# Performance work log

Hardware: AMD Instinct MI355X
Metric: run time of the kernel (lower is better)

## Reference

```python
import jax, jax.numpy as jnp
import numpy as np

NB = 31      # num_bands
PD = 64      # processing_dim


def _conv(x, w, b, groups, pad):
    # x: NCHW, w: OIHW (I = in_channels/groups)
    y = jax.lax.conv_general_dilated(
        x, w, window_strides=(1, 1), padding=pad,
        feature_group_count=groups,
        dimension_numbers=('NCHW', 'OIHW', 'NCHW'))
    return y + b[None, :, None, None]


def _gelu(z):
    # torch.nn.GELU() default is exact (erf-based)
    return jax.nn.gelu(z, approximate=False)


def setup_inputs() -> dict:
    key = jax.random.key(0)
    ks = jax.random.split(key, 11)
    s = 0.05
    inp = {
        'x':   jax.random.normal(ks[0], (2, NB, 192, 192), dtype=jnp.float32),
        # 31 independent band processors, stacked as grouped-conv weights (groups=31)
        'W1':  jax.random.normal(ks[1], (NB * PD, 1, 3, 3), dtype=jnp.float32) * s,
        'b1':  jax.random.normal(ks[2], (NB * PD,), dtype=jnp.float32) * s,
        'W2':  jax.random.normal(ks[3], (NB * PD, PD, 3, 3), dtype=jnp.float32) * s,
        'b2':  jax.random.normal(ks[4], (NB * PD,), dtype=jnp.float32) * s,
        'W3':  jax.random.normal(ks[5], (NB, PD, 1, 1), dtype=jnp.float32) * s,
        'b3':  jax.random.normal(ks[6], (NB,), dtype=jnp.float32) * s,
        # cross-band fusion 1x1 convs
        'Wf1': jax.random.normal(ks[7], (NB * 2, NB, 1, 1), dtype=jnp.float32) * s,
        'bf1': jax.random.normal(ks[8], (NB * 2,), dtype=jnp.float32) * s,
        'Wf2': jax.random.normal(ks[9], (NB, NB * 2, 1, 1), dtype=jnp.float32) * s,
        'bf2': jax.random.normal(ks[10], (NB,), dtype=jnp.float32) * s,
    }
    return inp


def reference(x, W1, b1, W2, b2, W3, b3, Wf1, bf1, Wf2, bf2):
    P3 = [(1, 1), (1, 1)]
    P1 = [(0, 0), (0, 0)]
    # per-band 3-layer stacks expressed as grouped convs (groups = num_bands)
    h = _gelu(_conv(x, W1, b1, NB, P3))           # [B, 31*64, H, W]
    h = _gelu(_conv(h, W2, b2, NB, P3))           # [B, 31*64, H, W]
    processed = _conv(h, W3, b3, NB, P1)          # [B, 31, H, W]
    # cross-band fusion
    f = _gelu(_conv(processed, Wf1, bf1, 1, P1))  # [B, 62, H, W]
    fused = _conv(f, Wf2, bf2, 1, P1)             # [B, 31, H, W]
    return x + fused
```

## Files before the change

kernel.cpp:

```cpp
#include <hip/hip_runtime.h>
#include <hip/hip_bf16.h>

#define NB 31
#define PD 64

typedef __attribute__((ext_vector_type(8))) short short8;
typedef __attribute__((ext_vector_type(16))) float f32x16;
typedef __attribute__((ext_vector_type(8))) int int8v;

__device__ __forceinline__ float gelu_f(float x) {
    float y = x * x;
    float p = __builtin_fmaf(y, __builtin_fmaf(y, 0.0042294f, -0.056913f), 0.395442f);
    float phi;
    asm("v_fma_f32 %0, %1, %2, 0.5 clamp" : "=v"(phi) : "v"(x), "v"(p));
    return x * phi;
}

__device__ __forceinline__ unsigned int cvt_pk_bf16(float lo, float hi) {
    unsigned int r;
    asm("v_cvt_pk_bf16_f32 %0, %1, %2" : "=v"(r) : "v"(lo), "v"(hi));
    return r;
}

__device__ __forceinline__ unsigned int pk_fp8(float a, float b) {
    return (unsigned int)__builtin_amdgcn_cvt_pk_fp8_f32(a, b, 0, false);
}

__device__ __forceinline__ int8v mk8(uint4 a, uint4 b) {
    int8v r;
    r[0] = a.x; r[1] = a.y; r[2] = a.z; r[3] = a.w;
    r[4] = b.x; r[5] = b.y; r[6] = b.z; r[7] = b.w;
    return r;
}

__global__ void prep_w2(const float* __restrict__ W2, unsigned char* __restrict__ W2s) {
    int e = blockIdx.x * 256 + threadIdx.x;
    const int TOT = NB * 2 * 9 * 64;
    if (e >= TOT) return;
    int lane = e & 63;
    int tap  = (e >> 6) % 9;
    int gh   = e / (9 * 64);
    int g = gh >> 1, oh = gh & 1;
    int col = lane & 31, hi = lane >> 5;
    const float* wp = W2 + ((size_t)(g * 64 + oh * 32 + col) * 64 + hi * 32) * 9 + tap;
    unsigned int d[8];
#pragma unroll
    for (int i = 0; i < 8; ++i) {
        float f0 = wp[(4 * i + 0) * 9];
        float f1 = wp[(4 * i + 1) * 9];
        float f2 = wp[(4 * i + 2) * 9];
        float f3 = wp[(4 * i + 3) * 9];
        d[i] = pk_fp8(f0, f1) | (pk_fp8(f2, f3) << 16);
    }
    uint4 q0, q1;
    q0.x = d[0]; q0.y = d[2]; q0.z = d[1]; q0.w = d[3];
    q1.x = d[4]; q1.y = d[6]; q1.z = d[5]; q1.w = d[7];
    uint4* op = (uint4*)W2s + (size_t)e * 2;
    op[0] = q0; op[1] = q1;
}

__global__ __launch_bounds__(512, 5) void band_kernel(
    const float* __restrict__ x, const float* __restrict__ W1, const float* __restrict__ b1,
    const float* __restrict__ b2, const float* __restrict__ W3, const float* __restrict__ b3,
    const unsigned char* __restrict__ W2s, float* __restrict__ out)
{
    __shared__ float xs[20 * 20];
    __shared__ uint4 h1s[352 * 5];
    __shared__ float outs[2 * 256];

    const int tid = threadIdx.x;
    const int tx = blockIdx.x % 12, ty = blockIdx.x / 12;
    const int g = blockIdx.y, n = blockIdx.z;
    const int x0 = tx * 16, y0 = ty * 16;

    const int lane = tid & 63;
    const int wid  = tid >> 6;
    const int w4   = wid & 3;
    const int oh   = wid >> 2;
    const int hi   = lane >> 5;
    const int col  = lane & 31;

    const float* xg = x + (size_t)(n * NB + g) * 192 * 192;
    if (tid < 400) {
        int r = tid / 20, c = tid - r * 20;
        int gy = y0 + r - 2, gx = x0 + c - 2;
        float v = 0.f;
        if (gy >= 0 && gy < 192 && gx >= 0 && gx < 192) v = xg[gy * 192 + gx];
        xs[tid] = v;
    }

    short8 a1;
    {
        const float* wp = W1 + (size_t)(g * 64 + oh * 32 + col) * 9;
        uint4 bw = {0u, 0u, 0u, 0u};
        if (hi == 0) {
            bw.x = cvt_pk_bf16(wp[0], wp[1]);
            bw.y = cvt_pk_bf16(wp[2], wp[3]);
            bw.z = cvt_pk_bf16(wp[4], wp[5]);
            bw.w = cvt_pk_bf16(wp[6], wp[7]);
        } else {
            bw.x = cvt_pk_bf16(wp[8], b1[g * 64 + oh * 32 + col]);
        }
        a1 = __builtin_bit_cast(short8, bw);
    }
    __syncthreads();

    char* h1c = (char*)h1s;
#pragma unroll
    for (int it = 0; it < 3; ++it) {
        const int t = w4 + 4 * it;
        if (t < 11) {
            const int posr = t * 32 + col;
            const int pos  = posr < 324 ? posr : 323;
            int py = pos / 18, px = pos - py * 18;
            int gy = y0 + py - 1, gx = x0 + px - 1;
            unsigned int msk = (gy >= 0 && gy < 192 && gx >= 0 && gx < 192) ? 0xFFFFFFFFu : 0u;

            uint4 bw = {0u, 0u, 0u, 0u};
            if (hi == 0) {
                float xv[8];
#pragma unroll
                for (int j2 = 0; j2 < 8; ++j2)
                    xv[j2] = xs[(py + j2 / 3) * 20 + px + (j2 % 3)];
                bw.x = cvt_pk_bf16(xv[0], xv[1]);
                bw.y = cvt_pk_bf16(xv[2], xv[3]);
                bw.z = cvt_pk_bf16(xv[4], xv[5]);
                bw.w = cvt_pk_bf16(xv[6], xv[7]);
            } else {
                bw.x = cvt_pk_bf16(xs[(py + 2) * 20 + px + 2], 1.0f);
            }
            short8 bfrag = __builtin_bit_cast(short8, bw);

            f32x16 z = {};
            f32x16 c0 = __builtin_amdgcn_mfma_f32_32x32x16_bf16(a1, bfrag, z, 0, 0, 0);

            const int rowb = posr * 80;
#pragma unroll
            for (int p2 = 0; p2 < 2; ++p2) {
                const int s0 = 2 * p2, s1 = 2 * p2 + 1;
                float u0 = gelu_f(c0[4 * s0 + 0]);
                float u1 = gelu_f(c0[4 * s0 + 1]);
                float u2 = gelu_f(c0[4 * s0 + 2]);
                float u3 = gelu_f(c0[4 * s0 + 3]);
                float v0 = gelu_f(c0[4 * s1 + 0]);
                float v1 = gelu_f(c0[4 * s1 + 1]);
                float v2 = gelu_f(c0[4 * s1 + 2]);
                float v3 = gelu_f(c0[4 * s1 + 3]);
                uint2 st;
                st.x = (pk_fp8(u0, u1) | (pk_fp8(u2, u3) << 16)) & msk;
                st.y = (pk_fp8(v0, v1) | (pk_fp8(v2, v3) << 16)) & msk;
                *(uint2*)(h1c + rowb + ((2 * oh + p2) << 4) + (hi << 3)) = st;
            }
        }
    }
    __syncthreads();

    const int lhalf = (lane >> 4) & 1;
    const int pxl   = lane & 15;
    const int base0 = (4 * w4 + lhalf) * 18 + pxl;

    const int gh = g * 2 + oh;
    const uint4* ap = (const uint4*)W2s + (size_t)gh * 9 * 128 + lane * 2;

    f32x16 acc0, acc1;
    {
        const float* bp = b2 + g * 64 + oh * 32 + 4 * hi;
#pragma unroll
        for (int s = 0; s < 4; ++s) {
            float4 q = *(const float4*)(bp + 8 * s);
            acc0[4 * s + 0] = q.x; acc0[4 * s + 1] = q.y;
            acc0[4 * s + 2] = q.z; acc0[4 * s + 3] = q.w;
            acc1[4 * s + 0] = q.x; acc1[4 * s + 1] = q.y;
            acc1[4 * s + 2] = q.z; acc1[4 * s + 3] = q.w;
        }
    }

    uint4 Aq[3][2];
    Aq[0][0] = ap[0];   Aq[0][1] = ap[1];
    Aq[1][0] = ap[128]; Aq[1][1] = ap[129];

#pragma unroll
    for (int tap = 0; tap < 9; ++tap) {
        if (tap + 2 < 9) {
            Aq[(tap + 2) % 3][0] = ap[(tap + 2) * 128];
            Aq[(tap + 2) % 3][1] = ap[(tap + 2) * 128 + 1];
        }
        const int D = (tap / 3) * 18 + (tap % 3);
        const int p0 = base0 + D;
        const int p1 = p0 + 36;
        const char* r0 = h1c + p0 * 80 + (hi << 5);
        const char* r1 = h1c + p1 * 80 + (hi << 5);
        uint4 b0a = *(const uint4*)(r0);
        uint4 b0b = *(const uint4*)(r0 + 16);
        uint4 b1a = *(const uint4*)(r1);
        uint4 b1b = *(const uint4*)(r1 + 16);
        int8v A = mk8(Aq[tap % 3][0], Aq[tap % 3][1]);
        acc0 = __builtin_amdgcn_mfma_scale_f32_32x32x64_f8f6f4(
                   A, mk8(b0a, b0b), acc0, 0, 0, 0, 0x7F7F7F7F, 0, 0x7F7F7F7F);
        acc1 = __builtin_amdgcn_mfma_scale_f32_32x32x64_f8f6f4(
                   A, mk8(b1a, b1b), acc1, 0, 0, 0, 0x7F7F7F7F, 0, 0x7F7F7F7F);
    }

    float pa = 0.f, pb = 0.f;
    {
        const float* wp3 = W3 + g * 64 + oh * 32 + 4 * hi;
#pragma unroll
        for (int s = 0; s < 4; ++s) {
            float4 qa = *(const float4*)(wp3 + 8 * s);
            pa = __builtin_fmaf(qa.x, gelu_f(acc0[4 * s + 0]), pa);
            pa = __builtin_fmaf(qa.y, gelu_f(acc0[4 * s + 1]), pa);
            pa = __builtin_fmaf(qa.z, gelu_f(acc0[4 * s + 2]), pa);
            pa = __builtin_fmaf(qa.w, gelu_f(acc0[4 * s + 3]), pa);
            pb = __builtin_fmaf(qa.x, gelu_f(acc1[4 * s + 0]), pb);
            pb = __builtin_fmaf(qa.y, gelu_f(acc1[4 * s + 1]), pb);
            pb = __builtin_fmaf(qa.z, gelu_f(acc1[4 * s + 2]), pb);
            pb = __builtin_fmaf(qa.w, gelu_f(acc1[4 * s + 3]), pb);
        }
    }
    pa += __shfl_xor(pa, 32);
    pb += __shfl_xor(pb, 32);
    if (lane < 32) {
        outs[oh * 256 + w4 * 64 + lane]      = pa;
        outs[oh * 256 + w4 * 64 + 32 + lane] = pb;
    }
    __syncthreads();

    if (tid < 256) {
        float v = outs[tid] + outs[256 + tid] + b3[g];
        int py = 4 * (tid >> 6) + 2 * ((tid >> 5) & 1) + ((tid >> 4) & 1);
        int px = tid & 15;
        out[((size_t)(n * NB + g) * 192 + y0 + py) * 192 + x0 + px] = v;
    }
}

__global__ __launch_bounds__(256) void fuse_kernel(
    const float* __restrict__ x,
    const float* __restrict__ Wf1, const float* __restrict__ bf1,
    const float* __restrict__ Wf2, const float* __restrict__ bf2,
    float* __restrict__ out)
{
    const int tid = threadIdx.x;
    int p = blockIdx.x * 256 + tid;
    int nn = p / 36864, pix = p - nn * 36864;
    float* basep = out + (size_t)nn * NB * 36864 + pix;
    const float* xb = x + (size_t)nn * NB * 36864 + pix;

    float v[31];
#pragma unroll
    for (int c = 0; c < 31; ++c) v[c] = basep[(size_t)c * 36864];

    float fused[31];
#pragma unroll
    for (int c = 0; c < 31; ++c) fused[c] = bf2[c];

#pragma unroll 2
    for (int j = 0; j < 62; ++j) {
        float a = bf1[j];
#pragma unroll
        for (int c = 0; c < 31; ++c) a = __builtin_fmaf(Wf1[j * 31 + c], v[c], a);
        float fj = gelu_f(a);
#pragma unroll
        for (int c = 0; c < 31; ++c) fused[c] = __builtin_fmaf(Wf2[c * 62 + j], fj, fused[c]);
    }
#pragma unroll
    for (int c = 0; c < 31; ++c) basep[(size_t)c * 36864] = xb[(size_t)c * 36864] + fused[c];
}

extern "C" void kernel_launch(void* const* d_in, const int* in_sizes, int n_in,
                              void* d_out, int out_size, void* d_ws, size_t ws_size,
                              hipStream_t stream) {
    const float* x   = (const float*)d_in[0];
    const float* W1  = (const float*)d_in[1];
    const float* b1  = (const float*)d_in[2];
    const float* W2  = (const float*)d_in[3];
    const float* b2  = (const float*)d_in[4];
    const float* W3  = (const float*)d_in[5];
    const float* b3  = (const float*)d_in[6];
    const float* Wf1 = (const float*)d_in[7];
    const float* bf1 = (const float*)d_in[8];
    const float* Wf2 = (const float*)d_in[9];
    const float* bf2 = (const float*)d_in[10];
    float* out = (float*)d_out;
    unsigned char* W2s = (unsigned char*)d_ws;

    const int TOT = NB * 2 * 9 * 64;
    hipLaunchKernelGGL(prep_w2, dim3((TOT + 255) / 256), dim3(256), 0, stream, W2, W2s);
    hipLaunchKernelGGL(band_kernel, dim3(144, NB, 2), dim3(512), 0, stream,
                       x, W1, b1, b2, W3, b3, W2s, out);
    hipLaunchKernelGGL(fuse_kernel, dim3(288), dim3(256), 0, stream,
                       x, Wf1, bf1, Wf2, bf2, out);
}
```

Measured before the change: 177.7 us.

## Give each wave all output channels for one position pair, dropping cross-wave reduction

Restructures the second-conv work split. Each wave now computes both 32-channel halves of the 64 output channels for a single 32-pixel group, reusing one B fragment from shared memory across two MFMAs instead of sharing one A fragment across two pixel groups. This lets each wave finish the W3 projection for its own pixels and write output directly, removing the outs shared buffer, a __syncthreads, and the cross-wave sum. The W2 fragment packing and the h1 store layout change to match, and the h1 store becomes a single 16-byte write. In exchange each wave loads twice the weight data per tap, and the weight prefetch ring is gone.

```diff
diff --git a/kernel.cpp b/kernel.cpp
--- a/kernel.cpp
+++ b/kernel.cpp
@@ -53,8 +53,8 @@
         d[i] = pk_fp8(f0, f1) | (pk_fp8(f2, f3) << 16);
     }
     uint4 q0, q1;
-    q0.x = d[0]; q0.y = d[2]; q0.z = d[1]; q0.w = d[3];
-    q1.x = d[4]; q1.y = d[6]; q1.z = d[5]; q1.w = d[7];
+    q0.x = d[0]; q0.y = d[2]; q0.z = d[4]; q0.w = d[6];
+    q1.x = d[1]; q1.y = d[3]; q1.z = d[5]; q1.w = d[7];
     uint4* op = (uint4*)W2s + (size_t)e * 2;
     op[0] = q0; op[1] = q1;
 }
@@ -66,7 +66,6 @@
 {
     __shared__ float xs[20 * 20];
     __shared__ uint4 h1s[352 * 5];
-    __shared__ float outs[2 * 256];
 
     const int tid = threadIdx.x;
     const int tx = blockIdx.x % 12, ty = blockIdx.x / 12;
@@ -134,102 +133,90 @@
             f32x16 z = {};
             f32x16 c0 = __builtin_amdgcn_mfma_f32_32x32x16_bf16(a1, bfrag, z, 0, 0, 0);
 
-            const int rowb = posr * 80;
-#pragma unroll
-            for (int p2 = 0; p2 < 2; ++p2) {
-                const int s0 = 2 * p2, s1 = 2 * p2 + 1;
-                float u0 = gelu_f(c0[4 * s0 + 0]);
-                float u1 = gelu_f(c0[4 * s0 + 1]);
-                float u2 = gelu_f(c0[4 * s0 + 2]);
-                float u3 = gelu_f(c0[4 * s0 + 3]);
-                float v0 = gelu_f(c0[4 * s1 + 0]);
-                float v1 = gelu_f(c0[4 * s1 + 1]);
-                float v2 = gelu_f(c0[4 * s1 + 2]);
-                float v3 = gelu_f(c0[4 * s1 + 3]);
-                uint2 st;
+            uint4 st;
+            {
+                float u0 = gelu_f(c0[0]),  u1 = gelu_f(c0[1]);
+                float u2 = gelu_f(c0[2]),  u3 = gelu_f(c0[3]);
                 st.x = (pk_fp8(u0, u1) | (pk_fp8(u2, u3) << 16)) & msk;
-                st.y = (pk_fp8(v0, v1) | (pk_fp8(v2, v3) << 16)) & msk;
-                *(uint2*)(h1c + rowb + ((2 * oh + p2) << 4) + (hi << 3)) = st;
-            }
+            }
+            {
+                float u0 = gelu_f(c0[4]),  u1 = gelu_f(c0[5]);
+                float u2 = gelu_f(c0[6]),  u3 = gelu_f(c0[7]);
+                st.y = (pk_fp8(u0, u1) | (pk_fp8(u2, u3) << 16)) & msk;
+            }
+            {
+                float u0 = gelu_f(c0[8]),  u1 = gelu_f(c0[9]);
+                float u2 = gelu_f(c0[10]), u3 = gelu_f(c0[11]);
+                st.z = (pk_fp8(u0, u1) | (pk_fp8(u2, u3) << 16)) & msk;
+            }
+            {
+                float u0 = gelu_f(c0[12]), u1 = gelu_f(c0[13]);
+                float u2 = gelu_f(c0[14]), u3 = gelu_f(c0[15]);
+                st.w = (pk_fp8(u0, u1) | (pk_fp8(u2, u3) << 16)) & msk;
+            }
+            *(uint4*)(h1c + posr * 80 + (oh << 5) + (hi << 4)) = st;
         }
     }
     __syncthreads();
 
     const int lhalf = (lane >> 4) & 1;
     const int pxl   = lane & 15;
-    const int base0 = (4 * w4 + lhalf) * 18 + pxl;
-
-    const int gh = g * 2 + oh;
-    const uint4* ap = (const uint4*)W2s + (size_t)gh * 9 * 128 + lane * 2;
+    const int base0 = (2 * wid + lhalf) * 18 + pxl;
+
+    const uint4* ap0 = (const uint4*)W2s + (size_t)(g * 2) * 9 * 128 + lane * 2;
+    const uint4* ap1 = ap0 + 9 * 128;
 
     f32x16 acc0, acc1;
     {
-        const float* bp = b2 + g * 64 + oh * 32 + 4 * hi;
+        const float* bp = b2 + g * 64 + 4 * hi;
 #pragma unroll
         for (int s = 0; s < 4; ++s) {
-            float4 q = *(const float4*)(bp + 8 * s);
-            acc0[4 * s + 0] = q.x; acc0[4 * s + 1] = q.y;
-            acc0[4 * s + 2] = q.z; acc0[4 * s + 3] = q.w;
-            acc1[4 * s + 0] = q.x; acc1[4 * s + 1] = q.y;
-            acc1[4 * s + 2] = q.z; acc1[4 * s + 3] = q.w;
-        }
-    }
-
-    uint4 Aq[3][2];
-    Aq[0][0] = ap[0];   Aq[0][1] = ap[1];
-    Aq[1][0] = ap[128]; Aq[1][1] = ap[129];
+            float4 q0 = *(const float4*)(bp + 8 * s);
+            float4 q1 = *(const float4*)(bp + 32 + 8 * s);
+            acc0[4 * s + 0] = q0.x; acc0[4 * s + 1] = q0.y;
+            acc0[4 * s + 2] = q0.z; acc0[4 * s + 3] = q0.w;
+            acc1[4 * s + 0] = q1.x; acc1[4 * s + 1] = q1.y;
+            acc1[4 * s + 2] = q1.z; acc1[4 * s + 3] = q1.w;
+        }
+    }
 
 #pragma unroll
     for (int tap = 0; tap < 9; ++tap) {
-        if (tap + 2 < 9) {
-            Aq[(tap + 2) % 3][0] = ap[(tap + 2) * 128];
-            Aq[(tap + 2) % 3][1] = ap[(tap + 2) * 128 + 1];
-        }
         const int D = (tap / 3) * 18 + (tap % 3);
         const int p0 = base0 + D;
-        const int p1 = p0 + 36;
         const char* r0 = h1c + p0 * 80 + (hi << 5);
-        const char* r1 = h1c + p1 * 80 + (hi << 5);
-        uint4 b0a = *(const uint4*)(r0);
-        uint4 b0b = *(const uint4*)(r0 + 16);
-        uint4 b1a = *(const uint4*)(r1);
-        uint4 b1b = *(const uint4*)(r1 + 16);
-        int8v A = mk8(Aq[tap % 3][0], Aq[tap % 3][1]);
+        uint4 ba = *(const uint4*)(r0);
+        uint4 bb = *(const uint4*)(r0 + 16);
+        int8v B = mk8(ba, bb);
+        uint4 a0l = ap0[tap * 128], a0h = ap0[tap * 128 + 1];
+        uint4 a1l = ap1[tap * 128], a1h = ap1[tap * 128 + 1];
         acc0 = __builtin_amdgcn_mfma_scale_f32_32x32x64_f8f6f4(
-                   A, mk8(b0a, b0b), acc0, 0, 0, 0, 0x7F7F7F7F, 0, 0x7F7F7F7F);
+                   mk8(a0l, a0h), B, acc0, 0, 0, 0, 0x7F7F7F7F, 0, 0x7F7F7F7F);
         acc1 = __builtin_amdgcn_mfma_scale_f32_32x32x64_f8f6f4(
-                   A, mk8(b1a, b1b), acc1, 0, 0, 0, 0x7F7F7F7F, 0, 0x7F7F7F7F);
-    }
-
-    float pa = 0.f, pb = 0.f;
+                   mk8(a1l, a1h), B, acc1, 0, 0, 0, 0x7F7F7F7F, 0, 0x7F7F7F7F);
+    }
+
+    float pa = 0.f;
     {
-        const float* wp3 = W3 + g * 64 + oh * 32 + 4 * hi;
+        const float* wp3 = W3 + g * 64 + 4 * hi;
 #pragma unroll
         for (int s = 0; s < 4; ++s) {
             float4 qa = *(const float4*)(wp3 + 8 * s);
+            float4 qb = *(const float4*)(wp3 + 32 + 8 * s);
             pa = __builtin_fmaf(qa.x, gelu_f(acc0[4 * s + 0]), pa);
             pa = __builtin_fmaf(qa.y, gelu_f(acc0[4 * s + 1]), pa);
             pa = __builtin_fmaf(qa.z, gelu_f(acc0[4 * s + 2]), pa);
             pa = __builtin_fmaf(qa.w, gelu_f(acc0[4 * s + 3]), pa);
-            pb = __builtin_fmaf(qa.x, gelu_f(acc1[4 * s + 0]), pb);
-            pb = __builtin_fmaf(qa.y, gelu_f(acc1[4 * s + 1]), pb);
-            pb = __builtin_fmaf(qa.z, gelu_f(acc1[4 * s + 2]), pb);
-            pb = __builtin_fmaf(qa.w, gelu_f(acc1[4 * s + 3]), pb);
+            pa = __builtin_fmaf(qb.x, gelu_f(acc1[4 * s + 0]), pa);
+            pa = __builtin_fmaf(qb.y, gelu_f(acc1[4 * s + 1]), pa);
+            pa = __builtin_fmaf(qb.z, gelu_f(acc1[4 * s + 2]), pa);
+            pa = __builtin_fmaf(qb.w, gelu_f(acc1[4 * s + 3]), pa);
         }
     }
     pa += __shfl_xor(pa, 32);
-    pb += __shfl_xor(pb, 32);
     if (lane < 32) {
-        outs[oh * 256 + w4 * 64 + lane]      = pa;
-        outs[oh * 256 + w4 * 64 + 32 + lane] = pb;
-    }
-    __syncthreads();
-
-    if (tid < 256) {
-        float v = outs[tid] + outs[256 + tid] + b3[g];
-        int py = 4 * (tid >> 6) + 2 * ((tid >> 5) & 1) + ((tid >> 4) & 1);
-        int px = tid & 15;
-        out[((size_t)(n * NB + g) * 192 + y0 + py) * 192 + x0 + px] = v;
+        int row = 2 * wid + (lane >> 4);
+        out[((size_t)(n * NB + g) * 192 + y0 + row) * 192 + x0 + (lane & 15)] = pa + b3[g];
     }
 }
 
```

Measured after the change: 190.8 us. 7.4% more time.

## Repack h1 into 16-byte LDS stores and split fuse hidden units across two half-blocks

Applied to the files above, without the earlier changes.

Changes the fp8 packing order of W2 fragments and of the layer-1 activations in shared memory, so each lane writes one 16-byte store instead of two 8-byte stores. The intent is fewer LDS store instructions in the band kernel. The fuse kernel now uses 512 threads per block. Each half computes 31 of the 62 hidden units for the same 256 pixels, and the two partial sums are combined through shared memory. This doubles parallelism in a kernel with only 288 blocks, at the cost of an extra barrier, shared-memory traffic, and 31 redundant input loads per pixel.

```diff
diff --git a/kernel.cpp b/kernel.cpp
--- a/kernel.cpp
+++ b/kernel.cpp
@@ -53,8 +53,8 @@
         d[i] = pk_fp8(f0, f1) | (pk_fp8(f2, f3) << 16);
     }
     uint4 q0, q1;
-    q0.x = d[0]; q0.y = d[2]; q0.z = d[1]; q0.w = d[3];
-    q1.x = d[4]; q1.y = d[6]; q1.z = d[5]; q1.w = d[7];
+    q0.x = d[0]; q0.y = d[2]; q0.z = d[4]; q0.w = d[6];
+    q1.x = d[1]; q1.y = d[3]; q1.z = d[5]; q1.w = d[7];
     uint4* op = (uint4*)W2s + (size_t)e * 2;
     op[0] = q0; op[1] = q1;
 }
@@ -134,23 +134,28 @@
             f32x16 z = {};
             f32x16 c0 = __builtin_amdgcn_mfma_f32_32x32x16_bf16(a1, bfrag, z, 0, 0, 0);
 
-            const int rowb = posr * 80;
-#pragma unroll
-            for (int p2 = 0; p2 < 2; ++p2) {
-                const int s0 = 2 * p2, s1 = 2 * p2 + 1;
-                float u0 = gelu_f(c0[4 * s0 + 0]);
-                float u1 = gelu_f(c0[4 * s0 + 1]);
-                float u2 = gelu_f(c0[4 * s0 + 2]);
-                float u3 = gelu_f(c0[4 * s0 + 3]);
-                float v0 = gelu_f(c0[4 * s1 + 0]);
-                float v1 = gelu_f(c0[4 * s1 + 1]);
-                float v2 = gelu_f(c0[4 * s1 + 2]);
-                float v3 = gelu_f(c0[4 * s1 + 3]);
-                uint2 st;
+            uint4 st;
+            {
+                float u0 = gelu_f(c0[0]),  u1 = gelu_f(c0[1]);
+                float u2 = gelu_f(c0[2]),  u3 = gelu_f(c0[3]);
                 st.x = (pk_fp8(u0, u1) | (pk_fp8(u2, u3) << 16)) & msk;
-                st.y = (pk_fp8(v0, v1) | (pk_fp8(v2, v3) << 16)) & msk;
-                *(uint2*)(h1c + rowb + ((2 * oh + p2) << 4) + (hi << 3)) = st;
-            }
+            }
+            {
+                float u0 = gelu_f(c0[4]),  u1 = gelu_f(c0[5]);
+                float u2 = gelu_f(c0[6]),  u3 = gelu_f(c0[7]);
+                st.y = (pk_fp8(u0, u1) | (pk_fp8(u2, u3) << 16)) & msk;
+            }
+            {
+                float u0 = gelu_f(c0[8]),  u1 = gelu_f(c0[9]);
+                float u2 = gelu_f(c0[10]), u3 = gelu_f(c0[11]);
+                st.z = (pk_fp8(u0, u1) | (pk_fp8(u2, u3) << 16)) & msk;
+            }
+            {
+                float u0 = gelu_f(c0[12]), u1 = gelu_f(c0[13]);
+                float u2 = gelu_f(c0[14]), u3 = gelu_f(c0[15]);
+                st.w = (pk_fp8(u0, u1) | (pk_fp8(u2, u3) << 16)) & msk;
+            }
+            *(uint4*)(h1c + posr * 80 + (oh << 5) + (hi << 4)) = st;
         }
     }
     __syncthreads();
@@ -233,14 +238,17 @@
     }
 }
 
-__global__ __launch_bounds__(256) void fuse_kernel(
+__global__ __launch_bounds__(512) void fuse_kernel(
     const float* __restrict__ x,
     const float* __restrict__ Wf1, const float* __restrict__ bf1,
     const float* __restrict__ Wf2, const float* __restrict__ bf2,
     float* __restrict__ out)
 {
-    const int tid = threadIdx.x;
-    int p = blockIdx.x * 256 + tid;
+    __shared__ float part[256 * 33];
+    const int tid  = threadIdx.x;
+    const int half = tid >> 8;
+    const int pixl = tid & 255;
+    int p = blockIdx.x * 256 + pixl;
     int nn = p / 36864, pix = p - nn * 36864;
     float* basep = out + (size_t)nn * NB * 36864 + pix;
     const float* xb = x + (size_t)nn * NB * 36864 + pix;
@@ -251,10 +259,10 @@
 
     float fused[31];
 #pragma unroll
-    for (int c = 0; c < 31; ++c) fused[c] = bf2[c];
-
-#pragma unroll 2
-    for (int j = 0; j < 62; ++j) {
+    for (int c = 0; c < 31; ++c) fused[c] = 0.f;
+
+    for (int jj = 0; jj < 31; ++jj) {
+        int j = half * 31 + jj;
         float a = bf1[j];
 #pragma unroll
         for (int c = 0; c < 31; ++c) a = __builtin_fmaf(Wf1[j * 31 + c], v[c], a);
@@ -262,8 +270,18 @@
 #pragma unroll
         for (int c = 0; c < 31; ++c) fused[c] = __builtin_fmaf(Wf2[c * 62 + j], fj, fused[c]);
     }
-#pragma unroll
-    for (int c = 0; c < 31; ++c) basep[(size_t)c * 36864] = xb[(size_t)c * 36864] + fused[c];
+
+    if (half == 1) {
+#pragma unroll
+        for (int c = 0; c < 31; ++c) part[pixl * 33 + c] = fused[c];
+    }
+    __syncthreads();
+    if (half == 0) {
+#pragma unroll
+        for (int c = 0; c < 31; ++c)
+            basep[(size_t)c * 36864] =
+                xb[(size_t)c * 36864] + fused[c] + part[pixl * 33 + c] + bf2[c];
+    }
 }
 
 extern "C" void kernel_launch(void* const* d_in, const int* in_sizes, int n_in,
@@ -287,6 +305,6 @@
     hipLaunchKernelGGL(prep_w2, dim3((TOT + 255) / 256), dim3(256), 0, stream, W2, W2s);
     hipLaunchKernelGGL(band_kernel, dim3(144, NB, 2), dim3(512), 0, stream,
                        x, W1, b1, b2, W3, b3, W2s, out);
-    hipLaunchKernelGGL(fuse_kernel, dim3(288), dim3(256), 0, stream,
+    hipLaunchKernelGGL(fuse_kernel, dim3(288), dim3(512), 0, stream,
                        x, Wf1, bf1, Wf2, bf2, out);
 }
```

Result: slower. 230.6 us (+29.8%).
